# Kernel tuning notes

Measured on AMD Instinct MI355X. Metric: run time of the kernel, lower is better.

Reference implementation:

```python
import jax, jax.numpy as jnp
import numpy as np

B, A, N_OBS, HX, N_ACT = 8192, 32, 128, 64, 16

def setup_inputs() -> dict:
    key = jax.random.key(0)
    ks = jax.random.split(key, 12)
    s = lambda *shape: 0.05 * jax.random.normal(ks[setup_inputs.i], shape, dtype=jnp.float32)
    out = {}
    setup_inputs.i = 0
    def nxt(*shape):
        setup_inputs.i += 1
        return 0.05 * jax.random.normal(ks[setup_inputs.i], shape, dtype=jnp.float32)
    out['obs'] = jax.random.normal(ks[0], (B, A, N_OBS), dtype=jnp.float32)
    out['W1'] = nxt(A, N_OBS, 128); out['b1'] = nxt(A, 128)
    out['W2'] = nxt(A, 128, HX);   out['b2'] = nxt(A, HX)
    out['Wg'] = nxt(A, HX, 2);     out['bg'] = nxt(A, 2)
    out['Wc'] = nxt(A, 2 * HX, HX); out['bc'] = nxt(A, HX)
    out['Wd'] = nxt(A, HX, N_ACT); out['bd'] = nxt(A, N_ACT)
    out['comm_mask'] = jax.random.randint(jax.random.fold_in(key, 99), (A, A), 0, 2, dtype=jnp.int32)
    return out

def reference(obs, W1, b1, W2, b2, Wg, bg, Wc, bc, Wd, bd, comm_mask):
    # encode: per-agent 2-layer MLP, batched over agents via einsum
    x = jax.nn.relu(jnp.einsum('ban,anh->bah', obs, W1) + b1)      # [B,A,128]
    h = jax.nn.relu(jnp.einsum('bah,ahk->bak', x, W2) + b2)        # [B,A,HX]
    # gate: Linear->ReLU->Softmax (computed as in original; only used via the
    # host-side RNG in the torch code, externalized here as comm_mask)
    gates = jax.nn.softmax(jax.nn.relu(jnp.einsum('bak,akg->bag', h, Wg) + bg), axis=-1)
    # communication: for agent i, mean of hidden states of communicating j != i
    mask = comm_mask.astype(h.dtype) * (1.0 - jnp.eye(A, dtype=h.dtype))  # [A_i, A_j]
    total = jnp.einsum('ij,bjk->bik', mask, h)                      # [B,A,HX]
    count = mask.sum(axis=1)                                        # [A]
    comm = total / jnp.maximum(count, 1.0)[None, :, None]           # count==0 -> zeros
    comm_in = jnp.concatenate([h, comm], axis=-1)                   # [B,A,2*HX]
    h2 = jnp.tanh(jnp.einsum('bac,ack->bak', comm_in, Wc) + bc)     # [B,A,HX]
    q = jnp.einsum('bak,akn->ban', h2, Wd) + bd                     # [B,A,N_ACT]
    return q
```

## Files before the change

kernel.cpp:

```cpp
#include <hip/hip_runtime.h>


#define NB   8192
#define NA   32
#define NOBS 128
#define NH1  128
#define HXX  64
#define NACT 16

typedef _Float16 half8 __attribute__((ext_vector_type(8)));
typedef _Float16 half4 __attribute__((ext_vector_type(4)));
typedef float    floatx4 __attribute__((ext_vector_type(4)));

#define MFMA16(af, bf, c) __builtin_amdgcn_mfma_f32_16x16x32_f16((af), (bf), (c), 0, 0, 0)

#define HWS_OFF 0
#define W1P_OFF (NB * NA * HXX)
#define W1P_CNT (NA * 8 * 4 * 512)
#define W2P_OFF (W1P_OFF + W1P_CNT)
#define W2P_CNT (NA * 4 * 4 * 512)
#define WCP_OFF (W2P_OFF + W2P_CNT)
#define WCP_CNT (NA * 4 * 4 * 512)
#define WDP_OFF (WCP_OFF + WCP_CNT)
#define WDP_CNT (NA * 1 * 2 * 512)
#define MN_OFF  (WDP_OFF + WDP_CNT)
#define PACK_TOTAL (W1P_CNT + W2P_CNT + WCP_CNT + WDP_CNT)

#define HSTR 2056
#define DEC_LDS (16 * HSTR * 2)

#define ENC_ROWS_BLK 512
#define ENC_TILES    8
#define ENC_SLAB     16384
#define ENC_LDS      (4 * ENC_SLAB)

using gas1p = const __attribute__((address_space(1))) void*;
using las3p = __attribute__((address_space(3))) void*;

__device__ __forceinline__ float fast_tanh(float x) {
    x = fminf(fmaxf(x, -10.f), 10.f);
    float e2 = __expf(2.f * x);
    return (e2 - 1.f) / (e2 + 1.f);
}

extern "C" __global__ void pack_kernel(const float* __restrict__ W1,
                                       const float* __restrict__ W2,
                                       const float* __restrict__ Wc,
                                       const float* __restrict__ Wd,
                                       const int*   __restrict__ cmask,
                                       _Float16* __restrict__ ws)
{
    int e = blockIdx.x * 256 + threadIdx.x;
    if (e >= PACK_TOTAL + NA * NA) return;
    if (e >= PACK_TOTAL) {
        int r = e - PACK_TOTAL, i = r >> 5, j = r & 31;
        int c = 0;
        for (int jj = 0; jj < NA; ++jj) c += (jj != i && cmask[i * NA + jj]) ? 1 : 0;
        float v = 0.f;
        if (j != i && cmask[i * NA + j]) v = 1.0f / (float)(c > 1 ? c : 1);
        ((float*)(ws + MN_OFF))[r] = v;
        return;
    }
    const float* src; _Float16* dst; int K, N, NT, NS, r;
    if (e < W1P_CNT) {
        src = W1; dst = ws + W1P_OFF; K = 128; N = 128; NT = 8; NS = 4; r = e;
    } else if (e < W1P_CNT + W2P_CNT) {
        src = W2; dst = ws + W2P_OFF; K = 128; N = 64; NT = 4; NS = 4; r = e - W1P_CNT;
    } else if (e < W1P_CNT + W2P_CNT + WCP_CNT) {
        src = Wc; dst = ws + WCP_OFF; K = 128; N = 64; NT = 4; NS = 4; r = e - W1P_CNT - W2P_CNT;
    } else {
        src = Wd; dst = ws + WDP_OFF; K = 64; N = 16; NT = 1; NS = 2; r = e - W1P_CNT - W2P_CNT - WCP_CNT;
    }
    int j = r & 7, l = (r >> 3) & 63;
    int rest = r >> 9;
    int s  = rest % NS; rest /= NS;
    int nt = rest % NT; rest /= NT;
    int a  = rest;
    int k = s * 32 + (l >> 4) * 8 + j;
    int n = nt * 16 + (l & 15);
    dst[r] = (_Float16)src[((size_t)a * K + k) * N + n];
}

extern "C" __global__ __launch_bounds__(256, 2)
void enc_kernel(const float* __restrict__ obs,
                const float* __restrict__ b1,
                const float* __restrict__ b2,
                const _Float16* __restrict__ W1p,
                const _Float16* __restrict__ W2p,
                _Float16* __restrict__ hws)
{
    extern __shared__ char smem[];

    const int tid  = threadIdx.x;
    const int a    = blockIdx.y;
    const int w    = tid >> 6, l = tid & 63;
    const int lm   = l & 15, lq = l >> 4;
    const int hrow = l >> 5;
    const int cch  = l & 31;
    char* SB = smem + w * ENC_SLAB;

    const int rowb = blockIdx.x * ENC_ROWS_BLK + w * 16;

    float b1v[8], b2v[4];
    #pragma unroll
    for (int nt = 0; nt < 8; ++nt) b1v[nt] = b1[a * NH1 + nt * 16 + lm];
    #pragma unroll
    for (int nt = 0; nt < 4; ++nt) b2v[nt] = b2[a * HXX + nt * 16 + lm];

    auto issue = [&](int t, int q) {
        #pragma unroll
        for (int i = 0; i < 8; ++i) {
            const int r = 2 * i + hrow;
            const int g = cch ^ (r & 7);
            const float* gp = obs + ((size_t)(rowb + t * 64 + r) * NA + a) * NOBS + g * 4;
            __builtin_amdgcn_global_load_lds((gas1p)gp,
                                             (las3p)(SB + q * 8192 + i * 1024),
                                             16, 0, 0);
        }
    };

    int p = 0;
    issue(0, 0);

    #pragma unroll 2
    for (int t = 0; t < ENC_TILES; ++t) {
        if (t < ENC_TILES - 1) {
            asm volatile("s_waitcnt lgkmcnt(0)" ::: "memory");
            issue(t + 1, p ^ 1);
            asm volatile("s_waitcnt vmcnt(8)" ::: "memory");
        } else {
            asm volatile("s_waitcnt vmcnt(0)" ::: "memory");
        }
        __builtin_amdgcn_sched_barrier(0);

        const char* SBp = SB + p * 8192;
        _Float16*   X   = (_Float16*)(SB + p * 8192);
        const int   rx  = lm & 7;

        floatx4 acc1[8];
        #pragma unroll
        for (int nt = 0; nt < 8; ++nt) acc1[nt] = (floatx4){0.f, 0.f, 0.f, 0.f};
        #pragma unroll
        for (int s = 0; s < 4; ++s) {
            const int c0 = s * 8 + lq * 2;
            floatx4 f0 = *(const floatx4*)(SBp + lm * 512 + (((c0    ) ^ rx) << 4));
            floatx4 f1 = *(const floatx4*)(SBp + lm * 512 + (((c0 + 1) ^ rx) << 4));
            half8 af;
            af[0] = (_Float16)f0[0]; af[1] = (_Float16)f0[1];
            af[2] = (_Float16)f0[2]; af[3] = (_Float16)f0[3];
            af[4] = (_Float16)f1[0]; af[5] = (_Float16)f1[1];
            af[6] = (_Float16)f1[2]; af[7] = (_Float16)f1[3];
            #pragma unroll
            for (int nt = 0; nt < 8; ++nt) {
                half8 bf = *(const half8*)&W1p[(((a * 8 + nt) * 4 + s) * 512) + l * 8];
                acc1[nt] = MFMA16(af, bf, acc1[nt]);
            }
        }
        #pragma unroll
        for (int nt = 0; nt < 8; ++nt)
            #pragma unroll
            for (int v = 0; v < 4; ++v) {
                float xv = fmaxf(acc1[nt][v] + b1v[nt], 0.f);
                X[(lq * 4 + v) * 136 + nt * 16 + lm] = (_Float16)xv;
            }

        floatx4 acc2[4];
        #pragma unroll
        for (int nt = 0; nt < 4; ++nt) acc2[nt] = (floatx4){0.f, 0.f, 0.f, 0.f};
        #pragma unroll
        for (int s = 0; s < 4; ++s) {
            half8 af2 = *(const half8*)&X[lm * 136 + s * 32 + lq * 8];
            #pragma unroll
            for (int nt = 0; nt < 4; ++nt) {
                half8 bf = *(const half8*)&W2p[(((a * 4 + nt) * 4 + s) * 512) + l * 8];
                acc2[nt] = MFMA16(af2, bf, acc2[nt]);
            }
        }
        #pragma unroll
        for (int nt = 0; nt < 4; ++nt)
            #pragma unroll
            for (int v = 0; v < 4; ++v) {
                float hv = fmaxf(acc2[nt][v] + b2v[nt], 0.f);
                X[(lq * 4 + v) * 136 + nt * 16 + lm] = (_Float16)hv;
            }

        {
            const int rr = l >> 2, cc = l & 3;
            #pragma unroll
            for (int q2 = 0; q2 < 2; ++q2) {
                const int chunk = cc + 4 * q2;
                half8 hv8 = *(const half8*)&X[rr * 136 + chunk * 8];
                *(half8*)&hws[((size_t)(rowb + t * 64 + rr) * NA + a) * HXX + chunk * 8] = hv8;
            }
        }
        p ^= 1;
    }
}

extern "C" __global__ __launch_bounds__(512)
void dec_kernel(const _Float16* __restrict__ hws,
                const float* __restrict__ MnG,
                const float* __restrict__ bc,
                const float* __restrict__ bd,
                const _Float16* __restrict__ Wcp,
                const _Float16* __restrict__ Wdp,
                float* __restrict__ out)
{
    extern __shared__ char smem[];
    _Float16* H = (_Float16*)smem;

    const int t  = threadIdx.x;
    const int b0 = blockIdx.x * 16;

    {
        const uint4* src = (const uint4*)(hws + (size_t)b0 * NA * HXX);
        #pragma unroll
        for (int it = 0; it < 8; ++it) {
            int idx = it * 512 + t;
            int row = idx >> 8, rem = idx & 255;
            *(uint4*)&H[row * HSTR + rem * 8] = src[idx];
        }
    }
    __syncthreads();

    const int w = t >> 6, l = t & 63, lm = l & 15, lq = l >> 4;

    half8 hacc[4][2];
    #pragma unroll
    for (int g = 0; g < 4; ++g)
        #pragma unroll
        for (int sb = 0; sb < 2; ++sb)
            #pragma unroll
            for (int q = 0; q < 8; ++q) hacc[g][sb][q] = (_Float16)0.f;

    #pragma unroll 4
    for (int j = 0; j < NA; ++j) {
        half8 v0 = *(const half8*)&H[lm * HSTR + j * 64 + lq * 8];
        half8 v1 = *(const half8*)&H[lm * HSTR + j * 64 + 32 + lq * 8];
        #pragma unroll
        for (int g = 0; g < 4; ++g) {
            int ag = __builtin_amdgcn_readfirstlane(w * 4 + g);
            _Float16 mh = (_Float16)MnG[ag * NA + j];
            hacc[g][0] += v0 * mh;
            hacc[g][1] += v1 * mh;
        }
    }
    __syncthreads();

    half4 h2r[4][4];
    #pragma unroll
    for (int nt = 0; nt < 4; ++nt) {
        floatx4 acc[4];
        #pragma unroll
        for (int g = 0; g < 4; ++g) acc[g] = (floatx4){0.f, 0.f, 0.f, 0.f};
        #pragma unroll
        for (int s = 0; s < 4; ++s) {
            #pragma unroll
            for (int g = 0; g < 4; ++g) {
                int ag = w * 4 + g;
                half8 af = (s < 2)
                    ? *(const half8*)&H[lm * HSTR + ag * 64 + s * 32 + lq * 8]
                    : hacc[g][s - 2];
                half8 bf = *(const half8*)&Wcp[(((ag * 4 + nt) * 4 + s) * 512) + l * 8];
                acc[g] = MFMA16(af, bf, acc[g]);
            }
        }
        #pragma unroll
        for (int g = 0; g < 4; ++g) {
            int ag = w * 4 + g;
            float bcv = bc[ag * HXX + nt * 16 + lm];
            #pragma unroll
            for (int v = 0; v < 4; ++v)
                h2r[g][nt][v] = (_Float16)fast_tanh(acc[g][v] + bcv);
        }
    }

    #pragma unroll
    for (int g = 0; g < 4; ++g) {
        int ag = w * 4 + g;
        #pragma unroll
        for (int nt = 0; nt < 4; ++nt)
            #pragma unroll
            for (int v = 0; v < 4; ++v)
                H[(lq * 4 + v) * HSTR + ag * 64 + nt * 16 + lm] = h2r[g][nt][v];
    }

    floatx4 acc3[4];
    #pragma unroll
    for (int g = 0; g < 4; ++g) acc3[g] = (floatx4){0.f, 0.f, 0.f, 0.f};
    #pragma unroll
    for (int s = 0; s < 2; ++s) {
        #pragma unroll
        for (int g = 0; g < 4; ++g) {
            int ag = w * 4 + g;
            half8 af = *(const half8*)&H[lm * HSTR + ag * 64 + s * 32 + lq * 8];
            half8 bf = *(const half8*)&Wdp[((ag * 2 + s) * 512) + l * 8];
            acc3[g] = MFMA16(af, bf, acc3[g]);
        }
    }

    #pragma unroll
    for (int g = 0; g < 4; ++g) {
        int ag = w * 4 + g;
        float bdv = bd[ag * NACT + lm];
        #pragma unroll
        for (int v = 0; v < 4; ++v) {
            int row = lq * 4 + v;
            out[((size_t)(b0 + row) * NA + ag) * NACT + lm] = acc3[g][v] + bdv;
        }
    }
}

extern "C" void kernel_launch(void* const* d_in, const int* in_sizes, int n_in,
                              void* d_out, int out_size, void* d_ws, size_t ws_size,
                              hipStream_t stream)
{
    const float* obs = (const float*)d_in[0];
    const float* W1  = (const float*)d_in[1];
    const float* b1  = (const float*)d_in[2];
    const float* W2  = (const float*)d_in[3];
    const float* b2  = (const float*)d_in[4];
    const float* Wc  = (const float*)d_in[7];
    const float* bc  = (const float*)d_in[8];
    const float* Wd  = (const float*)d_in[9];
    const float* bd  = (const float*)d_in[10];
    const int*   cm  = (const int*)d_in[11];

    float*    outp = (float*)d_out;
    _Float16* ws   = (_Float16*)d_ws;

    _Float16* hws = ws + HWS_OFF;
    _Float16* W1p = ws + W1P_OFF;
    _Float16* W2p = ws + W2P_OFF;
    _Float16* Wcp = ws + WCP_OFF;
    _Float16* Wdp = ws + WDP_OFF;
    const float* MnG = (const float*)(ws + MN_OFF);

    hipLaunchKernelGGL(pack_kernel, dim3((PACK_TOTAL + NA * NA + 255) / 256),
                       dim3(256), 0, stream, W1, W2, Wc, Wd, cm, ws);

    (void)hipFuncSetAttribute((const void*)enc_kernel,
                              hipFuncAttributeMaxDynamicSharedMemorySize, ENC_LDS);
    hipLaunchKernelGGL(enc_kernel, dim3(NB / ENC_ROWS_BLK, NA), dim3(256), ENC_LDS,
                       stream, obs, b1, b2, W1p, W2p, hws);

    (void)hipFuncSetAttribute((const void*)dec_kernel,
                              hipFuncAttributeMaxDynamicSharedMemorySize, DEC_LDS);
    hipLaunchKernelGGL(dec_kernel, dim3(NB / 16), dim3(512), DEC_LDS, stream,
                       hws, MnG, bc, bd, Wcp, Wdp, outp);
}
```

Baseline: 329.9 us.

## Hold encoder weights in registers and give each wave contiguous 256-row slabs

The encoder kernel now loads all W1/W2 MFMA B-fragments into registers once per wave instead of re-reading them from global memory on every tile. Each wave now handles a contiguous slab of 256 rows over 16 tiles, so a block covers 1024 rows and the grid shrinks. The DMA address offsets are precomputed and the waitcnt values are adjusted for the extra in-flight global loads. The cost is much higher register pressure (launch bounds drop to one block per CU) and fewer blocks to hide latency.

```diff
diff --git a/kernel.cpp b/kernel.cpp
--- a/kernel.cpp
+++ b/kernel.cpp
@@ -13,6 +13,7 @@
 typedef float    floatx4 __attribute__((ext_vector_type(4)));
 
 #define MFMA16(af, bf, c) __builtin_amdgcn_mfma_f32_16x16x32_f16((af), (bf), (c), 0, 0, 0)
+#define H8(x) __builtin_bit_cast(half8, (x))
 
 #define HWS_OFF 0
 #define W1P_OFF (NB * NA * HXX)
@@ -29,10 +30,11 @@
 #define HSTR 2056
 #define DEC_LDS (16 * HSTR * 2)
 
-#define ENC_ROWS_BLK 512
-#define ENC_TILES    8
-#define ENC_SLAB     16384
-#define ENC_LDS      (4 * ENC_SLAB)
+#define ENC_TILES 16
+#define ENC_WROWS 256
+#define ENC_BROWS 1024
+#define ENC_SLAB  16384
+#define ENC_LDS   (4 * ENC_SLAB)
 
 using gas1p = const __attribute__((address_space(1))) void*;
 using las3p = __attribute__((address_space(3))) void*;
@@ -81,7 +83,7 @@
     dst[r] = (_Float16)src[((size_t)a * K + k) * N + n];
 }
 
-extern "C" __global__ __launch_bounds__(256, 2)
+extern "C" __global__ __launch_bounds__(256, 1)
 void enc_kernel(const float* __restrict__ obs,
                 const float* __restrict__ b1,
                 const float* __restrict__ b2,
@@ -97,45 +99,75 @@
     const int lm   = l & 15, lq = l >> 4;
     const int hrow = l >> 5;
     const int cch  = l & 31;
-    char* SB = smem + w * ENC_SLAB;
-
-    const int rowb = blockIdx.x * ENC_ROWS_BLK + w * 16;
-
+    char* SBA = smem + w * ENC_SLAB;
+    char* SBB = SBA + 8192;
+
+    const int rowb = blockIdx.x * ENC_BROWS + w * ENC_WROWS;
+    const char* ob = (const char*)obs + (size_t)rowb * (NA * NOBS * 4) + (size_t)a * (NOBS * 4);
+
+    floatx4 w1r[8][4], w2r[4][4];
+    #pragma unroll
+    for (int nt = 0; nt < 8; ++nt)
+        #pragma unroll
+        for (int s = 0; s < 4; ++s)
+            w1r[nt][s] = *(const floatx4*)&W1p[(((a * 8 + nt) * 4 + s) * 512) + l * 8];
+    #pragma unroll
+    for (int nt = 0; nt < 4; ++nt)
+        #pragma unroll
+        for (int s = 0; s < 4; ++s)
+            w2r[nt][s] = *(const floatx4*)&W2p[(((a * 4 + nt) * 4 + s) * 512) + l * 8];
     float b1v[8], b2v[4];
     #pragma unroll
     for (int nt = 0; nt < 8; ++nt) b1v[nt] = b1[a * NH1 + nt * 16 + lm];
     #pragma unroll
     for (int nt = 0; nt < 4; ++nt) b2v[nt] = b2[a * HXX + nt * 16 + lm];
 
-    auto issue = [&](int t, int q) {
-        #pragma unroll
-        for (int i = 0; i < 8; ++i) {
-            const int r = 2 * i + hrow;
-            const int g = cch ^ (r & 7);
-            const float* gp = obs + ((size_t)(rowb + t * 64 + r) * NA + a) * NOBS + g * 4;
-            __builtin_amdgcn_global_load_lds((gas1p)gp,
-                                             (las3p)(SB + q * 8192 + i * 1024),
-                                             16, 0, 0);
-        }
+    #pragma unroll
+    for (int nt = 0; nt < 8; ++nt)
+        #pragma unroll
+        for (int s = 0; s < 4; ++s) asm volatile("" :: "v"(w1r[nt][s]));
+    #pragma unroll
+    for (int nt = 0; nt < 4; ++nt)
+        #pragma unroll
+        for (int s = 0; s < 4; ++s) asm volatile("" :: "v"(w2r[nt][s]));
+    #pragma unroll
+    for (int nt = 0; nt < 8; ++nt) asm volatile("" :: "v"(b1v[nt]));
+    #pragma unroll
+    for (int nt = 0; nt < 4; ++nt) asm volatile("" :: "v"(b2v[nt]));
+
+    int dmaoff[8];
+    #pragma unroll
+    for (int i = 0; i < 8; ++i) {
+        const int r = 2 * i + hrow;
+        dmaoff[i] = r * (NA * NOBS * 4) + ((cch ^ (r & 7)) << 4);
+    }
+
+    auto issue = [&](int t, char* dst) {
+        const char* bt = ob + (size_t)t * (16 * NA * NOBS * 4);
+        #pragma unroll
+        for (int i = 0; i < 8; ++i)
+            __builtin_amdgcn_global_load_lds((gas1p)(bt + dmaoff[i]),
+                                             (las3p)(dst + i * 1024), 16, 0, 0);
     };
 
-    int p = 0;
-    issue(0, 0);
-
-    #pragma unroll 2
+    issue(0, SBA);
+
     for (int t = 0; t < ENC_TILES; ++t) {
+        char* SBp = (t & 1) ? SBB : SBA;
+        char* SBn = (t & 1) ? SBA : SBB;
+
         if (t < ENC_TILES - 1) {
             asm volatile("s_waitcnt lgkmcnt(0)" ::: "memory");
-            issue(t + 1, p ^ 1);
-            asm volatile("s_waitcnt vmcnt(8)" ::: "memory");
+            issue(t + 1, SBn);
+            if (t == 0) asm volatile("s_waitcnt vmcnt(8)" ::: "memory");
+            else        asm volatile("s_waitcnt vmcnt(10)" ::: "memory");
         } else {
-            asm volatile("s_waitcnt vmcnt(0)" ::: "memory");
+            asm volatile("s_waitcnt vmcnt(2)" ::: "memory");
         }
         __builtin_amdgcn_sched_barrier(0);
 
-        const char* SBp = SB + p * 8192;
-        _Float16*   X   = (_Float16*)(SB + p * 8192);
-        const int   rx  = lm & 7;
+        _Float16* X = (_Float16*)SBp;
+        const int rx = lm & 7;
 
         floatx4 acc1[8];
         #pragma unroll
@@ -151,10 +183,8 @@
             af[4] = (_Float16)f1[0]; af[5] = (_Float16)f1[1];
             af[6] = (_Float16)f1[2]; af[7] = (_Float16)f1[3];
             #pragma unroll
-            for (int nt = 0; nt < 8; ++nt) {
-                half8 bf = *(const half8*)&W1p[(((a * 8 + nt) * 4 + s) * 512) + l * 8];
-                acc1[nt] = MFMA16(af, bf, acc1[nt]);
-            }
+            for (int nt = 0; nt < 8; ++nt)
+                acc1[nt] = MFMA16(af, H8(w1r[nt][s]), acc1[nt]);
         }
         #pragma unroll
         for (int nt = 0; nt < 8; ++nt)
@@ -171,10 +201,8 @@
         for (int s = 0; s < 4; ++s) {
             half8 af2 = *(const half8*)&X[lm * 136 + s * 32 + lq * 8];
             #pragma unroll
-            for (int nt = 0; nt < 4; ++nt) {
-                half8 bf = *(const half8*)&W2p[(((a * 4 + nt) * 4 + s) * 512) + l * 8];
-                acc2[nt] = MFMA16(af2, bf, acc2[nt]);
-            }
+            for (int nt = 0; nt < 4; ++nt)
+                acc2[nt] = MFMA16(af2, H8(w2r[nt][s]), acc2[nt]);
         }
         #pragma unroll
         for (int nt = 0; nt < 4; ++nt)
@@ -186,14 +214,14 @@
 
         {
             const int rr = l >> 2, cc = l & 3;
+            _Float16* hb = hws + ((size_t)(rowb + t * 16 + rr) * NA + a) * HXX;
             #pragma unroll
             for (int q2 = 0; q2 < 2; ++q2) {
                 const int chunk = cc + 4 * q2;
                 half8 hv8 = *(const half8*)&X[rr * 136 + chunk * 8];
-                *(half8*)&hws[((size_t)(rowb + t * 64 + rr) * NA + a) * HXX + chunk * 8] = hv8;
+                *(half8*)&hb[chunk * 8] = hv8;
             }
         }
-        p ^= 1;
     }
 }
 
@@ -341,7 +369,7 @@
 
     (void)hipFuncSetAttribute((const void*)enc_kernel,
                               hipFuncAttributeMaxDynamicSharedMemorySize, ENC_LDS);
-    hipLaunchKernelGGL(enc_kernel, dim3(NB / ENC_ROWS_BLK, NA), dim3(256), ENC_LDS,
+    hipLaunchKernelGGL(enc_kernel, dim3(NB / ENC_BROWS, NA), dim3(256), ENC_LDS,
                        stream, obs, b1, b2, W1p, W2p, hws);
 
     (void)hipFuncSetAttribute((const void*)dec_kernel,
```

New measurement: 271.7 us. -17.6%, faster.
